# Kernel optimization log

Hardware: AMD Instinct MI355X
Metric: run time of the kernel (lower is better)

The kernel has to match this reference:

```python
import jax, jax.numpy as jnp
import numpy as np

HIDDEN = 1024
HEADS = 16
DEPTH = HIDDEN // HEADS  # 64
B, F, T = 2, 2048, 2048


def setup_inputs() -> dict:
    key = jax.random.key(0)
    ks = jax.random.split(key, 7)
    return {
        "query_input": jax.random.normal(ks[0], (B, F, HIDDEN), dtype=jnp.float32),
        "source_input": jax.random.normal(ks[1], (B, T, HIDDEN), dtype=jnp.float32),
        "bias": jax.random.normal(ks[2], (1, 1, F, T), dtype=jnp.float32),
        "wq": jax.random.normal(ks[3], (HIDDEN, HEADS, DEPTH), dtype=jnp.float32) * 0.02,
        "wk": jax.random.normal(ks[4], (HIDDEN, HEADS, DEPTH), dtype=jnp.float32) * 0.02,
        "wv": jax.random.normal(ks[5], (HIDDEN, HEADS, DEPTH), dtype=jnp.float32) * 0.02,
        "wo": jax.random.normal(ks[6], (HEADS, DEPTH, HIDDEN), dtype=jnp.float32) * 0.02,
    }


def reference(query_input, source_input, bias, wq, wk, wv, wo):
    # projections: [B,S,C] x [C,N,H] -> [B,S,N,H]
    q = jnp.einsum("bfc,cnh->bfnh", query_input, wq)
    k = jnp.einsum("btc,cnh->btnh", source_input, wk)
    v = jnp.einsum("btc,cnh->btnh", source_input, wv)
    q = q * (DEPTH ** -0.5)
    # logits: [B,N,F,T], softmax over T (last dim)
    logits = jnp.einsum("btnh,bfnh->bnft", k, q)
    logits = logits + bias
    weights = jax.nn.softmax(logits, axis=3)
    attn = jnp.einsum("bnft,btnh->bfnh", weights, v)
    out = jnp.einsum("bfnh,nhe->bfe", attn, wo)
    return out
```

## Files before the change

kernel.cpp:

```cpp
#include <hip/hip_runtime.h>

#define LOG2E 1.44269504f

typedef __attribute__((ext_vector_type(8))) short short8v;
typedef __attribute__((ext_vector_type(4))) float f32x4;
typedef unsigned int u32;
typedef __attribute__((address_space(1))) const u32* gp_t;
typedef __attribute__((address_space(3))) u32* lp_t;

#define MFMA(a, b, c) __builtin_amdgcn_mfma_f32_16x16x32_bf16((a), (b), (c), 0, 0, 0)

__device__ __forceinline__ unsigned short f2bf(float f) {
  unsigned int u = __float_as_uint(f);
  u = (u + 0x7fffu + ((u >> 16) & 1u)) >> 16;
  return (unsigned short)u;
}
__device__ __forceinline__ u32 cvtpk(float lo, float hi) {
  u32 r;
  asm("v_cvt_pk_bf16_f32 %0, %1, %2" : "=v"(r) : "v"(lo), "v"(hi));
  return r;
}

__global__ void k_cvt(const float* __restrict__ in, unsigned short* __restrict__ out,
                      int n4, float scale) {
  int stride = gridDim.x * blockDim.x;
  for (int i = blockIdx.x * blockDim.x + threadIdx.x; i < n4; i += stride) {
    float4 v = reinterpret_cast<const float4*>(in)[i];
    ushort4 o;
    o.x = f2bf(v.x * scale); o.y = f2bf(v.y * scale);
    o.z = f2bf(v.z * scale); o.w = f2bf(v.w * scale);
    reinterpret_cast<ushort4*>(out)[i] = o;
  }
}

__global__ void k_cvt_t(const float* __restrict__ in, unsigned short* __restrict__ out,
                        float scale) {
  __shared__ float tile[32][33];
  int bx = blockIdx.x * 32, by = blockIdx.y * 32;
  int tx = threadIdx.x, ty = threadIdx.y;
  for (int r = ty; r < 32; r += 8)
    tile[r][tx] = in[(size_t)(by + r) * 1024 + bx + tx];
  __syncthreads();
  for (int r = ty; r < 32; r += 8)
    out[(size_t)(bx + r) * 1024 + by + tx] = f2bf(tile[tx][r] * scale);
}

__global__ void k_bias_perm(const float* __restrict__ in, float* __restrict__ out) {
  int bid = blockIdx.x;
  int fb = bid >> 5, ch = bid & 31;
  int tid = threadIdx.x;
  int tt = tid >> 6, rem = tid & 63;
  int g = rem >> 4, l15 = rem & 15;
  float4 v = *reinterpret_cast<const float4*>(
      &in[(size_t)(fb * 16 + l15) * 2048 + ch * 64 + tt * 16 + g * 4]);
  v.x *= LOG2E; v.y *= LOG2E; v.z *= LOG2E; v.w *= LOG2E;
  *reinterpret_cast<float4*>(&out[(size_t)bid * 1024 + tid * 4]) = v;
}

template <int TC, int MODE>
__global__ __launch_bounds__(256, 4)
void k_gemm(const unsigned short* __restrict__ A, const unsigned short* __restrict__ BT,
            void* __restrict__ dstv) {
  __shared__ __align__(16) unsigned short Al[2][4096];
  __shared__ __align__(16) unsigned short Bl[2][4096];
  const int tid = threadIdx.x;
  const int lane = tid & 63, wid = tid >> 6;
  const int g = lane >> 4, l15 = lane & 15, l7 = l15 & 7;
  const int wm = wid >> 1, wn = wid & 1;
  const int rowbase = blockIdx.y * 64, colbase = blockIdx.x * 64;
  const int xgl = (g ^ l7) << 4;

  const int jr = tid >> 3;
  const int sc = ((tid & 7) ^ (jr & 7)) << 3;
  const unsigned short* As0 = A + (size_t)(rowbase + jr) * 1024 + sc;
  const unsigned short* As1 = A + (size_t)(rowbase + jr + 32) * 1024 + sc;
  const unsigned short* Bs0 = BT + (size_t)(colbase + jr) * 1024 + sc;
  const unsigned short* Bs1 = BT + (size_t)(colbase + jr + 32) * 1024 + sc;

  const f32x4 zf = {0.f, 0.f, 0.f, 0.f};
  f32x4 acc[2][2];
  acc[0][0] = zf; acc[0][1] = zf; acc[1][0] = zf; acc[1][1] = zf;

  auto stage = [&](int buf, int k0) {
    char* Ad = (char*)&Al[buf][0];
    char* Bd = (char*)&Bl[buf][0];
    __builtin_amdgcn_global_load_lds((gp_t)(As0 + k0), (lp_t)(Ad + tid * 16), 16, 0, 0);
    __builtin_amdgcn_global_load_lds((gp_t)(As1 + k0), (lp_t)(Ad + 4096 + tid * 16), 16, 0, 0);
    __builtin_amdgcn_global_load_lds((gp_t)(Bs0 + k0), (lp_t)(Bd + tid * 16), 16, 0, 0);
    __builtin_amdgcn_global_load_lds((gp_t)(Bs1 + k0), (lp_t)(Bd + 4096 + tid * 16), 16, 0, 0);
  };
  auto compute = [&](int buf) {
    const char* Ac = (const char*)&Al[buf][0];
    const char* Bc = (const char*)&Bl[buf][0];
    __builtin_amdgcn_s_setprio(1);
#pragma unroll
    for (int kk = 0; kk < 2; ++kk) {
      short8v af[2], bfr[2];
#pragma unroll
      for (int mf = 0; mf < 2; ++mf)
        af[mf] = *reinterpret_cast<const short8v*>(
            Ac + ((wm * 32 + mf * 16 + l15) << 7) + (xgl ^ (kk << 6)));
#pragma unroll
      for (int nf = 0; nf < 2; ++nf)
        bfr[nf] = *reinterpret_cast<const short8v*>(
            Bc + ((wn * 32 + nf * 16 + l15) << 7) + (xgl ^ (kk << 6)));
#pragma unroll
      for (int mf = 0; mf < 2; ++mf)
#pragma unroll
        for (int nf = 0; nf < 2; ++nf)
          acc[mf][nf] = TC ? MFMA(bfr[nf], af[mf], acc[mf][nf])
                           : MFMA(af[mf], bfr[nf], acc[mf][nf]);
    }
    __builtin_amdgcn_s_setprio(0);
  };

  stage(0, 0);
  __syncthreads();
#pragma unroll 1
  for (int s = 0; s < 16; ++s) {
    if (s < 15) stage((s + 1) & 1, (s + 1) * 64);
    compute(s & 1);
    __syncthreads();
  }

#pragma unroll
  for (int mf = 0; mf < 2; ++mf)
#pragma unroll
    for (int nf = 0; nf < 2; ++nf) {
      f32x4 v = acc[mf][nf];
      if (MODE == 2) {
        int s = rowbase + wm * 32 + mf * 16 + l15;
        int c = colbase + wn * 32 + nf * 16 + g * 4;
        *reinterpret_cast<f32x4*>((float*)dstv + (size_t)s * 1024 + c) = v;
      } else if (MODE == 0) {
        int s = rowbase + wm * 32 + mf * 16 + l15;
        int c = colbase + wn * 32 + nf * 16 + g * 4;
        int b = s >> 11, s2 = s & 2047, hd = c >> 6, h = c & 63;
        uint2 w; w.x = cvtpk(v[0], v[1]); w.y = cvtpk(v[2], v[3]);
        *reinterpret_cast<uint2*>((unsigned short*)dstv +
            ((size_t)(b * 16 + hd) * 2048 + s2) * 64 + h) = w;
      } else {
        int s = rowbase + wm * 32 + mf * 16 + g * 4;
        int c = colbase + wn * 32 + nf * 16 + l15;
        int b = s >> 11, s2 = s & 2047, hd = c >> 6, h = c & 63;
        uint2 w; w.x = cvtpk(v[0], v[1]); w.y = cvtpk(v[2], v[3]);
        *reinterpret_cast<uint2*>((unsigned short*)dstv +
            ((size_t)(b * 16 + hd) * 64 + h) * 2048 + s2) = w;
      }
    }
}

__global__ __launch_bounds__(256, 4)
void k_attn(const unsigned short* __restrict__ qw,
            const unsigned short* __restrict__ kw,
            const unsigned short* __restrict__ vtw,
            const float* __restrict__ biaspf,
            unsigned short* __restrict__ attnb) {
  __shared__ __align__(16) unsigned short Kl[2][4096];
  __shared__ __align__(16) unsigned short Vl[2][4096];
  __shared__ __align__(16) unsigned short Pl[4][1024];

  const int tid = threadIdx.x;
  const int lane = tid & 63, wid = tid >> 6;
  const int g = lane >> 4, l15 = lane & 15, l7 = l15 & 7;
  const int xgl = (g ^ l7) << 4;

  const int bid = blockIdx.x;
  const int ft = bid >> 5, bn = bid & 31;
  const int b = bn >> 4, n = bn & 15;

  const size_t hoff = (size_t)bn * (2048 * 64);
  const unsigned short* qp = qw + hoff;
  const unsigned short* kp = kw + hoff;
  const unsigned short* vp = vtw + hoff;

  const int f0 = ft * 64 + wid * 16;
  const int fb = ft * 4 + wid;

  const int jr = tid >> 3;
  const int sc = ((tid & 7) ^ (jr & 7)) << 3;
  const unsigned short* Ks0 = kp + jr * 64 + sc;
  const unsigned short* Ks1 = kp + (jr + 32) * 64 + sc;
  const unsigned short* Vs0 = vp + jr * 2048 + sc;
  const unsigned short* Vs1 = vp + (jr + 32) * 2048 + sc;
  char* K0d = (char*)&Kl[0][0]; char* K1d = (char*)&Kl[1][0];
  char* V0d = (char*)&Vl[0][0]; char* V1d = (char*)&Vl[1][0];

  auto stage = [&](char* Kd, char* Vd, int ci) {
    int ko = ci << 12, vo = ci << 6;
    __builtin_amdgcn_global_load_lds((gp_t)(Ks0 + ko), (lp_t)(Kd + tid * 16), 16, 0, 0);
    __builtin_amdgcn_global_load_lds((gp_t)(Ks1 + ko), (lp_t)(Kd + 4096 + tid * 16), 16, 0, 0);
    __builtin_amdgcn_global_load_lds((gp_t)(Vs0 + vo), (lp_t)(Vd + tid * 16), 16, 0, 0);
    __builtin_amdgcn_global_load_lds((gp_t)(Vs1 + vo), (lp_t)(Vd + 4096 + tid * 16), 16, 0, 0);
  };

  short8v aq0 = *reinterpret_cast<const short8v*>(&qp[(size_t)(f0 + l15) * 64 + g * 8]);
  short8v aq1 = *reinterpret_cast<const short8v*>(&qp[(size_t)(f0 + l15) * 64 + 32 + g * 8]);

  const float* bias_lane = biaspf + (size_t)fb * 32768 + lane * 4;

  const f32x4 zf = {0.f, 0.f, 0.f, 0.f};
  f32x4 o[4];
  o[0] = zf; o[1] = zf; o[2] = zf; o[3] = zf;
  float ls = 0.f;
  char* Pbl = (char*)&Pl[wid][0] + l15 * 128;

  auto bload = [&](int ci, f32x4* bc) {
#pragma unroll
    for (int tt = 0; tt < 4; ++tt)
      bc[tt] = *reinterpret_cast<const f32x4*>(bias_lane + ci * 1024 + tt * 256);
  };

  auto compute = [&](const unsigned short* Kb, const unsigned short* Vb, const f32x4* bc) {
    const char* Kc = (const char*)Kb; const char* Vc = (const char*)Vb;
    f32x4 st[4];
    __builtin_amdgcn_s_setprio(1);
#pragma unroll
    for (int tt = 0; tt < 4; ++tt) {
      short8v kb0 = *reinterpret_cast<const short8v*>(Kc + ((tt * 16 + l15) << 7) + xgl);
      short8v kb1 = *reinterpret_cast<const short8v*>(Kc + ((tt * 16 + l15) << 7) + (xgl ^ 64));
      st[tt] = MFMA(kb1, aq1, MFMA(kb0, aq0, bc[tt]));
    }
    __builtin_amdgcn_s_setprio(0);

    float rs = 0.f;
#pragma unroll
    for (int tt = 0; tt < 4; ++tt) {
      float p0 = __builtin_amdgcn_exp2f(st[tt][0]);
      float p1 = __builtin_amdgcn_exp2f(st[tt][1]);
      float p2 = __builtin_amdgcn_exp2f(st[tt][2]);
      float p3 = __builtin_amdgcn_exp2f(st[tt][3]);
      rs += (p0 + p1) + (p2 + p3);
      uint2 w;
      w.x = cvtpk(p0, p1);
      w.y = cvtpk(p2, p3);
      *reinterpret_cast<uint2*>(Pbl + ((tt * 32 + g * 8) ^ (l7 * 16))) = w;
    }
    rs += __shfl_xor(rs, 16);
    rs += __shfl_xor(rs, 32);
    ls += rs;

    __builtin_amdgcn_s_setprio(1);
#pragma unroll
    for (int c = 0; c < 2; ++c) {
      short8v pa = *reinterpret_cast<const short8v*>(Pbl + ((c << 6) ^ xgl));
#pragma unroll
      for (int ht = 0; ht < 4; ++ht) {
        short8v vb = *reinterpret_cast<const short8v*>(
            Vc + ((ht * 16 + l15) << 7) + (xgl ^ (c << 6)));
        o[ht] = MFMA(pa, vb, o[ht]);
      }
    }
    __builtin_amdgcn_s_setprio(0);
  };

  f32x4 cb[4], nb[4];
  stage(K0d, V0d, 0);
  bload(0, cb);
  __syncthreads();
#pragma unroll 1
  for (int ci = 0; ci < 32; ci += 2) {
    stage(K1d, V1d, (ci + 1) & 31);
    bload((ci + 1) & 31, nb);
    compute(Kl[0], Vl[0], cb);
#pragma unroll
    for (int q = 0; q < 4; ++q) cb[q] = nb[q];
    __syncthreads();
    stage(K0d, V0d, (ci + 2) & 31);
    bload((ci + 2) & 31, nb);
    compute(Kl[1], Vl[1], cb);
#pragma unroll
    for (int q = 0; q < 4; ++q) cb[q] = nb[q];
    __syncthreads();
  }

  float inv = 1.f / ls;
  float i0 = __shfl(inv, g * 4 + 0, 16);
  float i1 = __shfl(inv, g * 4 + 1, 16);
  float i2 = __shfl(inv, g * 4 + 2, 16);
  float i3 = __shfl(inv, g * 4 + 3, 16);
#pragma unroll
  for (int ht = 0; ht < 4; ++ht) {
    unsigned short* ob = &attnb[((size_t)b * 2048 + f0 + g * 4) * 1024 + n * 64 + ht * 16 + l15];
    ob[0] = f2bf(o[ht][0] * i0);
    ob[1024] = f2bf(o[ht][1] * i1);
    ob[2048] = f2bf(o[ht][2] * i2);
    ob[3072] = f2bf(o[ht][3] * i3);
  }
}

extern "C" void kernel_launch(void* const* d_in, const int* in_sizes, int n_in,
                              void* d_out, int out_size, void* d_ws, size_t ws_size,
                              hipStream_t stream) {
  const float* query  = (const float*)d_in[0];
  const float* source = (const float*)d_in[1];
  const float* bias   = (const float*)d_in[2];
  const float* wq     = (const float*)d_in[3];
  const float* wk     = (const float*)d_in[4];
  const float* wv     = (const float*)d_in[5];
  const float* wo     = (const float*)d_in[6];

  char* ws = (char*)d_ws;
  unsigned short* qin_b  = (unsigned short*)(ws + 0);
  unsigned short* src_b  = (unsigned short*)(ws + 8388608);
  float*          bias_f = (float*)(ws + 0);
  unsigned short* wqT    = (unsigned short*)(ws + 16777216);
  unsigned short* wkT    = (unsigned short*)(ws + 18874368);
  unsigned short* wvT    = (unsigned short*)(ws + 20971520);
  unsigned short* woT    = (unsigned short*)(ws + 23068672);
  unsigned short* q_ws   = (unsigned short*)(ws + 25165824);
  unsigned short* k_ws   = (unsigned short*)(ws + 33554432);
  unsigned short* vT_ws  = (unsigned short*)(ws + 41943040);
  unsigned short* attn_b = (unsigned short*)(ws + 50331648);

  k_cvt<<<2048, 256, 0, stream>>>(query,  qin_b, 1048576, 1.0f);
  k_cvt<<<2048, 256, 0, stream>>>(source, src_b, 1048576, 1.0f);
  dim3 tb(32, 8);
  k_cvt_t<<<dim3(32, 32), tb, 0, stream>>>(wq, wqT, 0.125f * LOG2E);
  k_cvt_t<<<dim3(32, 32), tb, 0, stream>>>(wk, wkT, 1.0f);
  k_cvt_t<<<dim3(32, 32), tb, 0, stream>>>(wv, wvT, 1.0f);
  k_cvt_t<<<dim3(32, 32), tb, 0, stream>>>(wo, woT, 1.0f);

  k_gemm<1, 0><<<dim3(16, 64), 256, 0, stream>>>(qin_b, wqT, q_ws);
  k_gemm<1, 0><<<dim3(16, 64), 256, 0, stream>>>(src_b, wkT, k_ws);
  k_gemm<0, 1><<<dim3(16, 64), 256, 0, stream>>>(src_b, wvT, vT_ws);
  k_bias_perm<<<4096, 256, 0, stream>>>(bias, bias_f);
  k_attn<<<1024, 256, 0, stream>>>(q_ws, k_ws, vT_ws, bias_f, attn_b);
  k_gemm<1, 2><<<dim3(16, 64), 256, 0, stream>>>(attn_b, woT, d_out);
}
```

Before: 162.2 us.

## Fuse QKV projection GEMMs and batch conversion kernels into fewer launches

Merges the two activation-conversion kernels into one launch and the four weight-transpose kernels into one 3D-grid launch. Replaces the three separate Q/K/V projection GEMMs with a single k_gemmqkv kernel that uses 128x64 tiles over a concatenated weight matrix, picking the input and output layout per column block. The aim is to cut launch count and tail effects and to reuse each A tile across more columns. The cost is larger LDS use and more accumulators per thread, which may lower occupancy.

New measurement: 143.8 us. -11.4%, faster.

```diff
diff --git a/kernel.cpp b/kernel.cpp
--- a/kernel.cpp
+++ b/kernel.cpp
@@ -21,21 +21,29 @@
   return r;
 }
 
-__global__ void k_cvt(const float* __restrict__ in, unsigned short* __restrict__ out,
-                      int n4, float scale) {
+__global__ void k_cvt2(const float* __restrict__ a, const float* __restrict__ bsrc,
+                       unsigned short* __restrict__ oa, unsigned short* __restrict__ ob,
+                       int n4each) {
   int stride = gridDim.x * blockDim.x;
-  for (int i = blockIdx.x * blockDim.x + threadIdx.x; i < n4; i += stride) {
-    float4 v = reinterpret_cast<const float4*>(in)[i];
+  for (int i = blockIdx.x * blockDim.x + threadIdx.x; i < 2 * n4each; i += stride) {
+    bool second = i >= n4each;
+    int j = second ? i - n4each : i;
+    float4 v = second ? reinterpret_cast<const float4*>(bsrc)[j]
+                      : reinterpret_cast<const float4*>(a)[j];
     ushort4 o;
-    o.x = f2bf(v.x * scale); o.y = f2bf(v.y * scale);
-    o.z = f2bf(v.z * scale); o.w = f2bf(v.w * scale);
-    reinterpret_cast<ushort4*>(out)[i] = o;
-  }
-}
-
-__global__ void k_cvt_t(const float* __restrict__ in, unsigned short* __restrict__ out,
-                        float scale) {
+    o.x = f2bf(v.x); o.y = f2bf(v.y); o.z = f2bf(v.z); o.w = f2bf(v.w);
+    (second ? reinterpret_cast<ushort4*>(ob) : reinterpret_cast<ushort4*>(oa))[j] = o;
+  }
+}
+
+__global__ void k_cvt_t4(const float* __restrict__ w0, const float* __restrict__ w1,
+                         const float* __restrict__ w2, const float* __restrict__ w3,
+                         unsigned short* __restrict__ wqkvT, unsigned short* __restrict__ woT) {
   __shared__ float tile[32][33];
+  int z = blockIdx.z;
+  const float* in = (z == 0) ? w0 : (z == 1) ? w1 : (z == 2) ? w2 : w3;
+  unsigned short* out = (z < 3) ? (wqkvT + (size_t)z * 1048576) : woT;
+  float scale = (z == 0) ? 0.125f * LOG2E : 1.0f;
   int bx = blockIdx.x * 32, by = blockIdx.y * 32;
   int tx = threadIdx.x, ty = threadIdx.y;
   for (int r = ty; r < 32; r += 8)
@@ -55,6 +63,119 @@
       &in[(size_t)(fb * 16 + l15) * 2048 + ch * 64 + tt * 16 + g * 4]);
   v.x *= LOG2E; v.y *= LOG2E; v.z *= LOG2E; v.w *= LOG2E;
   *reinterpret_cast<float4*>(&out[(size_t)bid * 1024 + tid * 4]) = v;
+}
+
+__global__ __launch_bounds__(256)
+void k_gemmqkv(const unsigned short* __restrict__ Aq, const unsigned short* __restrict__ Asrc,
+               const unsigned short* __restrict__ W,
+               unsigned short* __restrict__ dq, unsigned short* __restrict__ dk,
+               unsigned short* __restrict__ dv) {
+  __shared__ __align__(16) unsigned short Al[2][8192];
+  __shared__ __align__(16) unsigned short Bl[2][4096];
+  const int tid = threadIdx.x;
+  const int lane = tid & 63, wid = tid >> 6;
+  const int g = lane >> 4, l15 = lane & 15, l7 = l15 & 7;
+  const int wm = wid >> 1, wn = wid & 1;
+  const int rowbase = blockIdx.y * 128;
+  const int colbase = blockIdx.x * 64;
+  const bool isV = colbase >= 2048;
+  const unsigned short* A = (colbase < 1024) ? Aq : Asrc;
+  const int xgl = (g ^ l7) << 4;
+
+  const int jr = tid >> 3;
+  const int sc = ((tid & 7) ^ (jr & 7)) << 3;
+  const unsigned short* As0 = A + (size_t)(rowbase + jr) * 1024 + sc;
+  const unsigned short* Ws0 = W + (size_t)(colbase + jr) * 1024 + sc;
+
+  const f32x4 zf = {0.f, 0.f, 0.f, 0.f};
+  f32x4 acc[4][2];
+#pragma unroll
+  for (int mf = 0; mf < 4; ++mf) { acc[mf][0] = zf; acc[mf][1] = zf; }
+
+  auto stage = [&](int buf, int k0) {
+    char* Ad = (char*)&Al[buf][0];
+    char* Bd = (char*)&Bl[buf][0];
+#pragma unroll
+    for (int p = 0; p < 4; ++p)
+      __builtin_amdgcn_global_load_lds((gp_t)(As0 + (size_t)p * 32 * 1024 + k0),
+                                       (lp_t)(Ad + (p * 256 + tid) * 16), 16, 0, 0);
+#pragma unroll
+    for (int p = 0; p < 2; ++p)
+      __builtin_amdgcn_global_load_lds((gp_t)(Ws0 + (size_t)p * 32 * 1024 + k0),
+                                       (lp_t)(Bd + (p * 256 + tid) * 16), 16, 0, 0);
+  };
+  auto ldfrags = [&](int buf, int kk, short8v af[4], short8v bfr[2]) {
+    const char* Ac = (const char*)&Al[buf][0];
+    const char* Bc = (const char*)&Bl[buf][0];
+#pragma unroll
+    for (int mf = 0; mf < 4; ++mf)
+      af[mf] = *reinterpret_cast<const short8v*>(
+          Ac + ((wm * 64 + mf * 16 + l15) << 7) + (xgl ^ (kk << 6)));
+#pragma unroll
+    for (int nf = 0; nf < 2; ++nf)
+      bfr[nf] = *reinterpret_cast<const short8v*>(
+          Bc + ((wn * 32 + nf * 16 + l15) << 7) + (xgl ^ (kk << 6)));
+  };
+
+  stage(0, 0);
+  __syncthreads();
+#pragma unroll 1
+  for (int s = 0; s < 16; ++s) {
+    if (s < 15) stage((s + 1) & 1, (s + 1) * 64);
+    __builtin_amdgcn_s_setprio(1);
+    if (!isV) {
+#pragma unroll
+      for (int kk = 0; kk < 2; ++kk) {
+        short8v af[4], bfr[2];
+        ldfrags(s & 1, kk, af, bfr);
+#pragma unroll
+        for (int mf = 0; mf < 4; ++mf)
+#pragma unroll
+          for (int nf = 0; nf < 2; ++nf) acc[mf][nf] = MFMA(bfr[nf], af[mf], acc[mf][nf]);
+      }
+    } else {
+#pragma unroll
+      for (int kk = 0; kk < 2; ++kk) {
+        short8v af[4], bfr[2];
+        ldfrags(s & 1, kk, af, bfr);
+#pragma unroll
+        for (int mf = 0; mf < 4; ++mf)
+#pragma unroll
+          for (int nf = 0; nf < 2; ++nf) acc[mf][nf] = MFMA(af[mf], bfr[nf], acc[mf][nf]);
+      }
+    }
+    __builtin_amdgcn_s_setprio(0);
+    __syncthreads();
+  }
+
+  if (!isV) {
+    unsigned short* dst = (colbase < 1024) ? dq : dk;
+    const int cb = colbase & 1023;
+#pragma unroll
+    for (int mf = 0; mf < 4; ++mf)
+#pragma unroll
+      for (int nf = 0; nf < 2; ++nf) {
+        f32x4 v = acc[mf][nf];
+        int s = rowbase + wm * 64 + mf * 16 + l15;
+        int c = cb + wn * 32 + nf * 16 + g * 4;
+        int b = s >> 11, s2 = s & 2047, hd = c >> 6, h = c & 63;
+        uint2 w; w.x = cvtpk(v[0], v[1]); w.y = cvtpk(v[2], v[3]);
+        *reinterpret_cast<uint2*>(dst + ((size_t)(b * 16 + hd) * 2048 + s2) * 64 + h) = w;
+      }
+  } else {
+    const int cb = colbase - 2048;
+#pragma unroll
+    for (int mf = 0; mf < 4; ++mf)
+#pragma unroll
+      for (int nf = 0; nf < 2; ++nf) {
+        f32x4 v = acc[mf][nf];
+        int s = rowbase + wm * 64 + mf * 16 + g * 4;
+        int c = cb + wn * 32 + nf * 16 + l15;
+        int b = s >> 11, s2 = s & 2047, hd = c >> 6, h = c & 63;
+        uint2 w; w.x = cvtpk(v[0], v[1]); w.y = cvtpk(v[2], v[3]);
+        *reinterpret_cast<uint2*>(dv + ((size_t)(b * 16 + hd) * 64 + h) * 2048 + s2) = w;
+      }
+  }
 }
 
 template <int TC, int MODE>
@@ -132,20 +253,6 @@
         int s = rowbase + wm * 32 + mf * 16 + l15;
         int c = colbase + wn * 32 + nf * 16 + g * 4;
         *reinterpret_cast<f32x4*>((float*)dstv + (size_t)s * 1024 + c) = v;
-      } else if (MODE == 0) {
-        int s = rowbase + wm * 32 + mf * 16 + l15;
-        int c = colbase + wn * 32 + nf * 16 + g * 4;
-        int b = s >> 11, s2 = s & 2047, hd = c >> 6, h = c & 63;
-        uint2 w; w.x = cvtpk(v[0], v[1]); w.y = cvtpk(v[2], v[3]);
-        *reinterpret_cast<uint2*>((unsigned short*)dstv +
-            ((size_t)(b * 16 + hd) * 2048 + s2) * 64 + h) = w;
-      } else {
-        int s = rowbase + wm * 32 + mf * 16 + g * 4;
-        int c = colbase + wn * 32 + nf * 16 + l15;
-        int b = s >> 11, s2 = s & 2047, hd = c >> 6, h = c & 63;
-        uint2 w; w.x = cvtpk(v[0], v[1]); w.y = cvtpk(v[2], v[3]);
-        *reinterpret_cast<uint2*>((unsigned short*)dstv +
-            ((size_t)(b * 16 + hd) * 64 + h) * 2048 + s2) = w;
       }
     }
 }
@@ -304,26 +411,18 @@
   unsigned short* qin_b  = (unsigned short*)(ws + 0);
   unsigned short* src_b  = (unsigned short*)(ws + 8388608);
   float*          bias_f = (float*)(ws + 0);
-  unsigned short* wqT    = (unsigned short*)(ws + 16777216);
-  unsigned short* wkT    = (unsigned short*)(ws + 18874368);
-  unsigned short* wvT    = (unsigned short*)(ws + 20971520);
+  unsigned short* wqkvT  = (unsigned short*)(ws + 16777216);
   unsigned short* woT    = (unsigned short*)(ws + 23068672);
   unsigned short* q_ws   = (unsigned short*)(ws + 25165824);
   unsigned short* k_ws   = (unsigned short*)(ws + 33554432);
   unsigned short* vT_ws  = (unsigned short*)(ws + 41943040);
   unsigned short* attn_b = (unsigned short*)(ws + 50331648);
 
-  k_cvt<<<2048, 256, 0, stream>>>(query,  qin_b, 1048576, 1.0f);
-  k_cvt<<<2048, 256, 0, stream>>>(source, src_b, 1048576, 1.0f);
+  k_cvt2<<<2048, 256, 0, stream>>>(query, source, qin_b, src_b, 1048576);
   dim3 tb(32, 8);
-  k_cvt_t<<<dim3(32, 32), tb, 0, stream>>>(wq, wqT, 0.125f * LOG2E);
-  k_cvt_t<<<dim3(32, 32), tb, 0, stream>>>(wk, wkT, 1.0f);
-  k_cvt_t<<<dim3(32, 32), tb, 0, stream>>>(wv, wvT, 1.0f);
-  k_cvt_t<<<dim3(32, 32), tb, 0, stream>>>(wo, woT, 1.0f);
-
-  k_gemm<1, 0><<<dim3(16, 64), 256, 0, stream>>>(qin_b, wqT, q_ws);
-  k_gemm<1, 0><<<dim3(16, 64), 256, 0, stream>>>(src_b, wkT, k_ws);
-  k_gemm<0, 1><<<dim3(16, 64), 256, 0, stream>>>(src_b, wvT, vT_ws);
+  k_cvt_t4<<<dim3(32, 32, 4), tb, 0, stream>>>(wq, wk, wv, wo, wqkvT, woT);
+
+  k_gemmqkv<<<dim3(48, 32), 256, 0, stream>>>(qin_b, src_b, wqkvT, q_ws, k_ws, vT_ws);
   k_bias_perm<<<4096, 256, 0, stream>>>(bias, bias_f);
   k_attn<<<1024, 256, 0, stream>>>(q_ws, k_ws, vT_ws, bias_f, attn_b);
   k_gemm<1, 2><<<dim3(16, 64), 256, 0, stream>>>(attn_b, woT, d_out);
```
